# Optimization experiments

Hardware: AMD Instinct MI355X
Metric: run time of the kernel (lower is better)

The kernel has to match this reference:

```python
import jax, jax.numpy as jnp
import numpy as np

B, H, W = 8, 1024, 1024
IN_DIM, HID, OUT_DIM = 8, 16, 3


def setup_inputs() -> dict:
    key = jax.random.key(0)
    ks = jax.random.split(key, 8)
    x = jax.random.uniform(ks[0], (B, H, W, IN_DIM), dtype=jnp.float32)
    mask = jax.random.randint(ks[1], (B, H, W), 0, 2).astype(jnp.bool_)
    # kaiming-uniform-ish hidden weights, xavier-ish last layer, zero biases
    w0 = jax.random.uniform(ks[2], (IN_DIM, HID), jnp.float32, -1.0, 1.0) * np.sqrt(6.0 / IN_DIM)
    b0 = jnp.zeros((HID,), jnp.float32)
    w1 = jax.random.uniform(ks[3], (HID, HID), jnp.float32, -1.0, 1.0) * np.sqrt(6.0 / HID)
    b1 = jnp.zeros((HID,), jnp.float32)
    w2 = jax.random.uniform(ks[4], (HID, OUT_DIM), jnp.float32, -1.0, 1.0) * np.sqrt(6.0 / (HID + OUT_DIM))
    b2 = jnp.zeros((OUT_DIM,), jnp.float32)
    return {"x": x, "mask": mask, "w0": w0, "b0": b0, "w1": w1, "b1": b1, "w2": w2, "b2": b2}


def reference(x, mask, w0, b0, w1, b1, w2, b2):
    # x: [B,H,W,IN_DIM]; mask: [B,H,W] bool
    rgb = x[..., :3]            # [B,H,W,3]
    res = x[..., 3:4]           # [B,H,W,1]
    # tiny 2-hidden-layer MLP with ReLU, sigmoid head (dense; masked rows zeroed after)
    h = jax.nn.relu(jnp.einsum('bhwi,ij->bhwj', x, w0) + b0)
    h = jax.nn.relu(jnp.einsum('bhwi,ij->bhwj', h, w1) + b1)
    y = jax.nn.sigmoid(jnp.einsum('bhwi,ij->bhwj', h, w2) + b2)  # [B,H,W,3]
    blended = (1.0 - res) * rgb + res * y
    # masked-out pixels are exactly zero, matching the torch scatter into zeros
    return jnp.where(mask[..., None], blended, jnp.zeros((), x.dtype))
```

## Files before the change

kernel.cpp:

```cpp
#include <hip/hip_runtime.h>

#define NPIX (8 * 1024 * 1024)
#define IN 8
#define HID 16
#define OUTC 3
#define BLK 256
#define PPT 2

typedef _Float16 f16x2 __attribute__((ext_vector_type(2)));

__device__ __forceinline__ f16x2 pkrtz(float lo, float hi) {
    return __builtin_bit_cast(f16x2, __builtin_amdgcn_cvt_pkrtz(lo, hi));
}

#define WS_W0H 16
#define WS_W1H 80
#define WS_W2H 208
#define WS_B0  240
#define WS_B1  256
#define WS_B2  272

__device__ __forceinline__ unsigned int pack2(float lo, float hi) {
    _Float16 a = (_Float16)lo, b = (_Float16)hi;
    unsigned short ua = __builtin_bit_cast(unsigned short, a);
    unsigned short ub = __builtin_bit_cast(unsigned short, b);
    return (unsigned int)ua | ((unsigned int)ub << 16);
}

__global__ void prep_kernel(const unsigned int* __restrict__ m,
                            const float* __restrict__ w0, const float* __restrict__ b0,
                            const float* __restrict__ w1, const float* __restrict__ b1,
                            const float* __restrict__ w2, const float* __restrict__ b2,
                            float* __restrict__ ws) {
    const int t = threadIdx.x;
    unsigned int* wsu = (unsigned int*)ws;
    if (t < 64) {
        unsigned int acc = 0u;
        #pragma unroll
        for (int k = 0; k < 8; ++k) acc |= m[t * 8 + k];
        const unsigned long long big = __ballot(acc > 1u);
        if (t == 0) ((int*)ws)[0] = big ? 1 : 0;
    }
    if (t < 64)  { int j = t >> 2, k = t & 3;
        wsu[WS_W0H + j * 4 + k] = pack2(w0[(2 * k) * HID + j], w0[(2 * k + 1) * HID + j]); }
    if (t < 128) { int j = t >> 3, k = t & 7;
        wsu[WS_W1H + j * 8 + k] = pack2(w1[(2 * k) * HID + j], w1[(2 * k + 1) * HID + j]); }
    if (t < 24)  { int j = t >> 3, k = t & 7;
        wsu[WS_W2H + j * 8 + k] = pack2(w2[(2 * k) * OUTC + j], w2[(2 * k + 1) * OUTC + j]); }
    if (t < HID)  { ws[WS_B0 + t] = b0[t]; ws[WS_B1 + t] = b1[t]; }
    if (t < OUTC) { ws[WS_B2 + t] = b2[t]; }
}

__global__ void __launch_bounds__(BLK, 4) colormlp_kernel(
    const float* __restrict__ x,
    const void*  __restrict__ mask,
    const float* __restrict__ ws,
    float* __restrict__ out)
{
    __shared__ __align__(16) float sOut[BLK * PPT * OUTC];

    const int t = threadIdx.x;
    const unsigned int* wsu = (const unsigned int*)ws;
    const int mflag = ((const int*)ws)[0];

    const unsigned int pix0 = (blockIdx.x * BLK + t) * PPT;

    float4 x0[PPT], x1[PPT];
    {
        const float4* xp = (const float4*)(x + (size_t)pix0 * IN);
        #pragma unroll
        for (int p = 0; p < PPT; ++p) { x0[p] = xp[2 * p]; x1[p] = xp[2 * p + 1]; }
    }

    f16x2 xh[PPT][4];
    #pragma unroll
    for (int p = 0; p < PPT; ++p) {
        xh[p][0] = pkrtz(x0[p].x, x0[p].y);
        xh[p][1] = pkrtz(x0[p].z, x0[p].w);
        xh[p][2] = pkrtz(x1[p].x, x1[p].y);
        xh[p][3] = pkrtz(x1[p].z, x1[p].w);
    }

    f16x2 h0h[PPT][HID / 2];
    {
        float h0[PPT][HID];
        #pragma unroll
        for (int j = 0; j < HID; ++j) {
            f16x2 w[4];
            #pragma unroll
            for (int k = 0; k < 4; ++k) w[k] = __builtin_bit_cast(f16x2, wsu[WS_W0H + j * 4 + k]);
            const float bj = ws[WS_B0 + j];
            #pragma unroll
            for (int p = 0; p < PPT; ++p) {
                float acc = bj;
                #pragma unroll
                for (int k = 0; k < 4; ++k) acc = __builtin_amdgcn_fdot2(xh[p][k], w[k], acc, false);
                h0[p][j] = fmaxf(acc, 0.0f);
            }
        }
        #pragma unroll
        for (int p = 0; p < PPT; ++p)
            #pragma unroll
            for (int i = 0; i < HID / 2; ++i)
                h0h[p][i] = pkrtz(h0[p][2 * i], h0[p][2 * i + 1]);
    }

    f16x2 h1h[PPT][HID / 2];
    {
        float h1[PPT][HID];
        #pragma unroll
        for (int j = 0; j < HID; ++j) {
            f16x2 w[8];
            #pragma unroll
            for (int k = 0; k < 8; ++k) w[k] = __builtin_bit_cast(f16x2, wsu[WS_W1H + j * 8 + k]);
            const float bj = ws[WS_B1 + j];
            #pragma unroll
            for (int p = 0; p < PPT; ++p) {
                float acc = bj;
                #pragma unroll
                for (int k = 0; k < 8; ++k) acc = __builtin_amdgcn_fdot2(h0h[p][k], w[k], acc, false);
                h1[p][j] = fmaxf(acc, 0.0f);
            }
        }
        #pragma unroll
        for (int p = 0; p < PPT; ++p)
            #pragma unroll
            for (int i = 0; i < HID / 2; ++i)
                h1h[p][i] = pkrtz(h1[p][2 * i], h1[p][2 * i + 1]);
    }

    int mv[PPT];
    if (mflag) {
        uchar2 m2 = *(const uchar2*)((const unsigned char*)mask + pix0);
        mv[0] = m2.x; mv[1] = m2.y;
    } else {
        int2 m2 = *(const int2*)((const int*)mask + pix0);
        mv[0] = m2.x; mv[1] = m2.y;
    }

    #pragma unroll
    for (int p = 0; p < PPT; ++p) {
        const float res = x0[p].w;
        float ov[OUTC];
        #pragma unroll
        for (int j = 0; j < OUTC; ++j) {
            float acc = ws[WS_B2 + j];
            #pragma unroll
            for (int k = 0; k < 8; ++k)
                acc = __builtin_amdgcn_fdot2(h1h[p][k],
                        __builtin_bit_cast(f16x2, wsu[WS_W2H + j * 8 + k]), acc, false);
            float e = __expf(-acc);
            float y = __builtin_amdgcn_rcpf(1.0f + e);
            float rgb = (j == 0) ? x0[p].x : (j == 1) ? x0[p].y : x0[p].z;
            float bl = fmaf(res, y - rgb, rgb);
            ov[j] = mv[p] ? bl : 0.0f;
        }
        float* sp = sOut + (size_t)(t * PPT + p) * OUTC;
        ((float2*)sp)[0] = make_float2(ov[0], ov[1]);
        sp[2] = ov[2];
    }
    __syncthreads();

    {
        const float4* s4 = (const float4*)sOut;
        float4* o4 = (float4*)(out + (size_t)blockIdx.x * (BLK * PPT * OUTC));
        o4[t] = s4[t];
        if (t < (BLK * PPT * OUTC) / 4 - BLK) o4[BLK + t] = s4[BLK + t];
    }
}

extern "C" void kernel_launch(void* const* d_in, const int* in_sizes, int n_in,
                              void* d_out, int out_size, void* d_ws, size_t ws_size,
                              hipStream_t stream) {
    const float* x    = (const float*)d_in[0];
    const void*  mask = d_in[1];
    const float* w0   = (const float*)d_in[2];
    const float* b0   = (const float*)d_in[3];
    const float* w1   = (const float*)d_in[4];
    const float* b1   = (const float*)d_in[5];
    const float* w2   = (const float*)d_in[6];
    const float* b2   = (const float*)d_in[7];
    float* out = (float*)d_out;
    float* ws  = (float*)d_ws;

    prep_kernel<<<1, BLK, 0, stream>>>((const unsigned int*)mask,
                                       w0, b0, w1, b1, w2, b2, ws);

    const int grid = NPIX / (BLK * PPT);
    colormlp_kernel<<<grid, BLK, 0, stream>>>(x, mask, ws, out);
}
```

Measured before the change: 431.1 us.

## Use persistent grid-stride loop with register double-buffered prefetch of inputs

Replaces the one-block-per-tile launch with a fixed 1024-block grid where each thread loops over pixel pairs. While one pair is being computed, the next pair's inputs and mask are already loading into registers. The LDS staging and __syncthreads for output are dropped in favor of direct float2 stores, and launch bounds drop to 3 waves per SIMD to make room for the extra registers. The risks are lower occupancy, less coalesced output stores, and too few blocks to keep all CUs busy and hide latency.

```diff
diff --git a/kernel.cpp b/kernel.cpp
--- a/kernel.cpp
+++ b/kernel.cpp
@@ -6,6 +6,8 @@
 #define OUTC 3
 #define BLK 256
 #define PPT 2
+#define GRID 1024
+#define NITER (NPIX / (GRID * BLK * PPT))
 
 typedef _Float16 f16x2 __attribute__((ext_vector_type(2)));
 
@@ -51,26 +53,14 @@
     if (t < OUTC) { ws[WS_B2 + t] = b2[t]; }
 }
 
-__global__ void __launch_bounds__(BLK, 4) colormlp_kernel(
-    const float* __restrict__ x,
-    const void*  __restrict__ mask,
-    const float* __restrict__ ws,
-    float* __restrict__ out)
+__device__ __forceinline__ void compute_store_pair(
+    const unsigned int* __restrict__ wsu, const float* __restrict__ ws,
+    float* __restrict__ out, unsigned int pr,
+    float4 x0a, float4 x1a, float4 x0b, float4 x1b, int ma, int mb)
 {
-    __shared__ __align__(16) float sOut[BLK * PPT * OUTC];
-
-    const int t = threadIdx.x;
-    const unsigned int* wsu = (const unsigned int*)ws;
-    const int mflag = ((const int*)ws)[0];
-
-    const unsigned int pix0 = (blockIdx.x * BLK + t) * PPT;
-
-    float4 x0[PPT], x1[PPT];
-    {
-        const float4* xp = (const float4*)(x + (size_t)pix0 * IN);
-        #pragma unroll
-        for (int p = 0; p < PPT; ++p) { x0[p] = xp[2 * p]; x1[p] = xp[2 * p + 1]; }
-    }
+    const float4 x0[PPT] = { x0a, x0b };
+    const float4 x1[PPT] = { x1a, x1b };
+    const int    mv[PPT] = { ma, mb };
 
     f16x2 xh[PPT][4];
     #pragma unroll
@@ -129,19 +119,10 @@
                 h1h[p][i] = pkrtz(h1[p][2 * i], h1[p][2 * i + 1]);
     }
 
-    int mv[PPT];
-    if (mflag) {
-        uchar2 m2 = *(const uchar2*)((const unsigned char*)mask + pix0);
-        mv[0] = m2.x; mv[1] = m2.y;
-    } else {
-        int2 m2 = *(const int2*)((const int*)mask + pix0);
-        mv[0] = m2.x; mv[1] = m2.y;
-    }
-
+    float ov[PPT][OUTC];
     #pragma unroll
     for (int p = 0; p < PPT; ++p) {
         const float res = x0[p].w;
-        float ov[OUTC];
         #pragma unroll
         for (int j = 0; j < OUTC; ++j) {
             float acc = ws[WS_B2 + j];
@@ -153,20 +134,61 @@
             float y = __builtin_amdgcn_rcpf(1.0f + e);
             float rgb = (j == 0) ? x0[p].x : (j == 1) ? x0[p].y : x0[p].z;
             float bl = fmaf(res, y - rgb, rgb);
-            ov[j] = mv[p] ? bl : 0.0f;
+            ov[p][j] = mv[p] ? bl : 0.0f;
         }
-        float* sp = sOut + (size_t)(t * PPT + p) * OUTC;
-        ((float2*)sp)[0] = make_float2(ov[0], ov[1]);
-        sp[2] = ov[2];
-    }
-    __syncthreads();
-
-    {
-        const float4* s4 = (const float4*)sOut;
-        float4* o4 = (float4*)(out + (size_t)blockIdx.x * (BLK * PPT * OUTC));
-        o4[t] = s4[t];
-        if (t < (BLK * PPT * OUTC) / 4 - BLK) o4[BLK + t] = s4[BLK + t];
-    }
+    }
+
+    float2* op = (float2*)(out + (size_t)pr * (PPT * OUTC));
+    op[0] = make_float2(ov[0][0], ov[0][1]);
+    op[1] = make_float2(ov[0][2], ov[1][0]);
+    op[2] = make_float2(ov[1][1], ov[1][2]);
+}
+
+__global__ void __launch_bounds__(BLK, 3) colormlp_kernel(
+    const float* __restrict__ x,
+    const void*  __restrict__ mask,
+    const float* __restrict__ ws,
+    float* __restrict__ out)
+{
+    const int t = threadIdx.x;
+    const unsigned int* wsu = (const unsigned int*)ws;
+    const int mflag = ((const int*)ws)[0];
+    const unsigned int stride = GRID * BLK;
+
+    unsigned int prA = blockIdx.x * BLK + t;
+
+    float4 A0a, A1a, A0b, A1b, B0a, B1a, B0b, B1b;
+    int mAa, mAb, mBa, mBb;
+
+    const float4* xp = (const float4*)x;
+
+#define LOADX(P0a, P1a, P0b, P1b, MA, MB, pr) do {                              \
+        const float4* _b = xp + (size_t)(pr) * 4;                               \
+        P0a = _b[0]; P1a = _b[1]; P0b = _b[2]; P1b = _b[3];                     \
+        if (mflag) {                                                            \
+            uchar2 _m = *(const uchar2*)((const unsigned char*)mask + (size_t)(pr) * 2); \
+            MA = _m.x; MB = _m.y;                                               \
+        } else {                                                                \
+            int2 _m = *(const int2*)((const int*)mask + (size_t)(pr) * 2);      \
+            MA = _m.x; MB = _m.y;                                               \
+        }                                                                       \
+    } while (0)
+
+    LOADX(A0a, A1a, A0b, A1b, mAa, mAb, prA);
+
+    #pragma unroll 1
+    for (int i = 0; i < NITER; i += 2) {
+        const unsigned int prB = prA + stride;
+        LOADX(B0a, B1a, B0b, B1b, mBa, mBb, prB);
+        compute_store_pair(wsu, ws, out, prA, A0a, A1a, A0b, A1b, mAa, mAb);
+
+        const unsigned int prA2 = prB + stride;
+        if (i + 2 < NITER)
+            LOADX(A0a, A1a, A0b, A1b, mAa, mAb, prA2);
+        compute_store_pair(wsu, ws, out, prB, B0a, B1a, B0b, B1b, mBa, mBb);
+        prA = prA2;
+    }
+#undef LOADX
 }
 
 extern "C" void kernel_launch(void* const* d_in, const int* in_sizes, int n_in,
@@ -186,6 +208,5 @@
     prep_kernel<<<1, BLK, 0, stream>>>((const unsigned int*)mask,
                                        w0, b0, w1, b1, w2, b2, ws);
 
-    const int grid = NPIX / (BLK * PPT);
-    colormlp_kernel<<<grid, BLK, 0, stream>>>(x, mask, ws, out);
-}
+    colormlp_kernel<<<GRID, BLK, 0, stream>>>(x, mask, ws, out);
+}
```

Result: slower. 441.4 us (+2.4%).
